# Optimization experiments

Measured on AMD Instinct MI355X. Metric: run time of the kernel, lower is better.

The kernel has to match this reference:

```python
import jax, jax.numpy as jnp
import numpy as np

N = 100000
IN_DIM = 128
HID = 64
OUT = 4


def _gcn_conv(x, W, b, src, dst, deg_inv_sqrt):
    """PyG GCNConv: linear transform, then symmetric-normalized scatter-add.
    src/dst already include self-loops; deg_inv_sqrt precomputed over them."""
    h = x @ W                                   # [N, H]
    norm = deg_inv_sqrt[src] * deg_inv_sqrt[dst]  # [E+N]
    msg = h[src] * norm[:, None]                # gather + scale, [E+N, H]
    out = jax.ops.segment_sum(msg, dst, num_segments=N)  # scatter-add
    return out + b


def setup_inputs() -> dict:
    key = jax.random.key(0)
    ks = jax.random.split(key, 8)
    E = 1600000
    x = jax.random.normal(ks[0], (N, IN_DIM), dtype=jnp.float32)
    edge_index = jax.random.randint(ks[1], (2, E), 0, N, dtype=jnp.int32)
    # Glorot-ish init for weights
    W1 = jax.random.normal(ks[2], (IN_DIM, HID), dtype=jnp.float32) / np.sqrt(IN_DIM)
    b1 = jnp.zeros((HID,), dtype=jnp.float32)
    W2 = jax.random.normal(ks[3], (HID, HID), dtype=jnp.float32) / np.sqrt(HID)
    b2 = jnp.zeros((HID,), dtype=jnp.float32)
    Wfc = jax.random.normal(ks[4], (HID, OUT), dtype=jnp.float32) / np.sqrt(HID)
    bfc = jnp.zeros((OUT,), dtype=jnp.float32)
    return {"x": x, "edge_index": edge_index, "W1": W1, "b1": b1,
            "W2": W2, "b2": b2, "Wfc": Wfc, "bfc": bfc}


def reference(x, edge_index, W1, b1, W2, b2, Wfc, bfc):
    # Add self-loops (GCNConv default add_self_loops=True)
    loops = jnp.arange(N, dtype=edge_index.dtype)
    src = jnp.concatenate([edge_index[0], loops])
    dst = jnp.concatenate([edge_index[1], loops])
    # Symmetric normalization: deg computed at aggregation targets (dst)
    deg = jax.ops.segment_sum(jnp.ones_like(dst, dtype=x.dtype), dst,
                              num_segments=N)
    deg_inv_sqrt = jnp.where(deg > 0, jax.lax.rsqrt(deg), 0.0)

    h = _gcn_conv(x, W1, b1, src, dst, deg_inv_sqrt)
    h = jax.nn.relu(h)                 # dropout is identity in eval mode
    h = _gcn_conv(h, W2, b2, src, dst, deg_inv_sqrt)
    h = jax.nn.relu(h)
    return h @ Wfc + bfc               # [N, 4]
```

## Files before the change

kernel.cpp:

```cpp
#include <hip/hip_runtime.h>
#include <hip/hip_fp16.h>


#define BCAP 5120
#define BINB 512
#define CHUNK 3200
#define CAP  64
#define LCAP 32

typedef float v2f __attribute__((ext_vector_type(2)));
typedef _Float16 f16x8 __attribute__((ext_vector_type(8)));
typedef float f32x4 __attribute__((ext_vector_type(4)));

__global__ __launch_bounds__(256) void k_bin_gemm1(
        const int* __restrict__ src, const int* __restrict__ dst, int e,
        int* bcur, unsigned* __restrict__ binned,
        const float* __restrict__ X, const float* __restrict__ W1,
        __half* __restrict__ Hh, int n) {
    __shared__ union {
        struct {
            unsigned ec[CHUNK];
            unsigned short eb[CHUNK];
            int lh[512], lbase[512], lr[512];
        } b;
        struct {
            _Float16 As[128 * 136];
            _Float16 Bs[64 * 136];
        } g;
    } sm;

    int t = threadIdx.x;

    if (blockIdx.x < BINB) {
        unsigned* ec = sm.b.ec;
        unsigned short* eb = sm.b.eb;
        int* lh = sm.b.lh; int* lbase = sm.b.lbase; int* lr = sm.b.lr;
        for (int i = t; i < 512; i += 256) { lh[i] = 0; lr[i] = 0; }
        __syncthreads();
        int chunk = (e + BINB - 1) / BINB;
        int lo = blockIdx.x * chunk;
        int hi = min(e, lo + chunk);
        for (int i = lo + t; i < hi; i += 256) {
            int d = dst[i];
            int b = d >> 8;
            ec[i - lo] = ((unsigned)src[i] << 8) | (unsigned)(d & 255);
            eb[i - lo] = (unsigned short)b;
            atomicAdd(&lh[b], 1);
        }
        __syncthreads();
        for (int i = t; i < 512; i += 256)
            lbase[i] = lh[i] ? atomicAdd(&bcur[i], lh[i]) : 0;
        __syncthreads();
        int cnt = hi - lo;
        for (int i = t; i < cnt; i += 256) {
            int b = eb[i];
            int r = lbase[b] + atomicAdd(&lr[b], 1);
            if (r < BCAP)
                binned[(size_t)b * BCAP + r] = ec[i];
        }
    } else {
        constexpr int K = 128, KP = 136;
        _Float16* As = sm.g.As;
        _Float16* Bs = sm.g.Bs;
        _Float16* H = (_Float16*)Hh;

        #pragma unroll
        for (int p = 0; p < 8; ++p) {
            int i = t + p * 256;
            int k = i >> 4, nn4 = (i & 15) << 2;
            float4 v = ((const float4*)W1)[i];
            Bs[(nn4 + 0) * KP + k] = (_Float16)v.x;
            Bs[(nn4 + 1) * KP + k] = (_Float16)v.y;
            Bs[(nn4 + 2) * KP + k] = (_Float16)v.z;
            Bs[(nn4 + 3) * KP + k] = (_Float16)v.w;
        }

        int row0 = (blockIdx.x - BINB) * 128;
        #pragma unroll
        for (int p = 0; p < 8; ++p) {
            int gi  = t + p * 256;
            int row = gi >> 4, sg = gi & 15;
            int grow = row0 + row;
            float4 v0 = make_float4(0.f, 0.f, 0.f, 0.f), v1 = v0;
            if (grow < n) {
                v0 = *(const float4*)(X + (size_t)grow * K + sg * 8);
                v1 = *(const float4*)(X + (size_t)grow * K + sg * 8 + 4);
            }
            union { __half2 h[4]; float4 f; } u;
            u.h[0] = __floats2half2_rn(v0.x, v0.y);
            u.h[1] = __floats2half2_rn(v0.z, v0.w);
            u.h[2] = __floats2half2_rn(v1.x, v1.y);
            u.h[3] = __floats2half2_rn(v1.z, v1.w);
            *(float4*)(As + row * KP + sg * 8) = u.f;
        }
        __syncthreads();

        int wv   = t >> 6;
        int lane = t & 63;
        int m    = lane & 15;
        int quad = lane >> 4;
        int r0   = wv * 32;

        f32x4 acc[2][4] = {};
        #pragma unroll
        for (int kb = 0; kb < K / 32; ++kb) {
            f16x8 af0 = *(const f16x8*)(As + (r0 + m) * KP + quad * 8 + kb * 32);
            f16x8 af1 = *(const f16x8*)(As + (r0 + 16 + m) * KP + quad * 8 + kb * 32);
            #pragma unroll
            for (int nt = 0; nt < 4; ++nt) {
                f16x8 bf = *(const f16x8*)(Bs + (nt * 16 + m) * KP + quad * 8 + kb * 32);
                acc[0][nt] = __builtin_amdgcn_mfma_f32_16x16x32_f16(af0, bf, acc[0][nt], 0, 0, 0);
                acc[1][nt] = __builtin_amdgcn_mfma_f32_16x16x32_f16(af1, bf, acc[1][nt], 0, 0, 0);
            }
        }

        #pragma unroll
        for (int mt = 0; mt < 2; ++mt) {
            int gr[4];
            #pragma unroll
            for (int r = 0; r < 4; ++r)
                gr[r] = row0 + r0 + mt * 16 + quad * 4 + r;
            #pragma unroll
            for (int nt = 0; nt < 4; ++nt)
                #pragma unroll
                for (int r = 0; r < 4; ++r) {
                    if (gr[r] < n)
                        H[(size_t)gr[r] * 64 + nt * 16 + m] =
                            (_Float16)acc[mt][nt][r];
                    else if (gr[r] == n)
                        H[(size_t)n * 64 + nt * 16 + m] = (_Float16)0.f;
                }
        }
    }
}

__global__ __launch_bounds__(256) void k_bucket2(const unsigned* __restrict__ binned,
                                                 const int* __restrict__ bcur,
                                                 int n, int* __restrict__ cnt,
                                                 int* __restrict__ slots) {
    __shared__ int lists[256 * (LCAP + 1)];
    __shared__ int lcnt[256];
    int b = blockIdx.x, t = threadIdx.x;
    int node0 = b << 8;
    size_t ebase = (size_t)b * BCAP;
    int ecnt = min(bcur[b], BCAP);
    lcnt[t] = 0;
    __syncthreads();
    for (int j = t; j < ecnt; j += 256) {
        unsigned ed = binned[ebase + j];
        int ld = ed & 255u;
        int s  = (int)(ed >> 8);
        int r  = atomicAdd(&lcnt[ld], 1);
        if (r < LCAP)
            lists[ld * (LCAP + 1) + r] = s;
        else if (r < CAP)
            slots[((size_t)(node0 + ld) << 6) + r] = s;
    }
    __syncthreads();
    int d = node0 + t;
    if (d < n) {
        int c = lcnt[t];
        cnt[d] = c;
        int m = min(c, LCAP);
        size_t base = (size_t)d << 6;
        for (int r = 0; r < m; ++r)
            slots[base + r] = lists[t * (LCAP + 1) + r];
    }
}

__global__ __launch_bounds__(256) void k_gemm2(const __half* __restrict__ X,
                                               const float* __restrict__ W2,
                                               const int* __restrict__ cnt,
                                               __half* __restrict__ Hh, int n) {
    constexpr int K = 64, KP = 72;
    __shared__ _Float16 As[128 * KP];
    __shared__ _Float16 Bs[64 * KP];

    int t = threadIdx.x;
    _Float16* H = (_Float16*)Hh;

    #pragma unroll
    for (int p = 0; p < 4; ++p) {
        int i = t + p * 256;
        int k = i >> 4, nn4 = (i & 15) << 2;
        float4 v = ((const float4*)W2)[i];
        Bs[(nn4 + 0) * KP + k] = (_Float16)v.x;
        Bs[(nn4 + 1) * KP + k] = (_Float16)v.y;
        Bs[(nn4 + 2) * KP + k] = (_Float16)v.z;
        Bs[(nn4 + 3) * KP + k] = (_Float16)v.w;
    }

    int row0 = blockIdx.x * 128;
    const __half* Xh = X;
    #pragma unroll
    for (int p = 0; p < 4; ++p) {
        int gi  = t + p * 256;
        int row = gi >> 3, sg = gi & 7;
        int grow = row0 + row;
        float4 v = make_float4(0.f, 0.f, 0.f, 0.f);
        if (grow < n)
            v = *(const float4*)(Xh + (size_t)grow * K + sg * 8);
        *(float4*)(As + row * KP + sg * 8) = v;
    }
    __syncthreads();

    int wv   = t >> 6;
    int lane = t & 63;
    int m    = lane & 15;
    int quad = lane >> 4;
    int r0   = wv * 32;

    f32x4 acc[2][4] = {};
    #pragma unroll
    for (int kb = 0; kb < K / 32; ++kb) {
        f16x8 af0 = *(const f16x8*)(As + (r0 + m) * KP + quad * 8 + kb * 32);
        f16x8 af1 = *(const f16x8*)(As + (r0 + 16 + m) * KP + quad * 8 + kb * 32);
        #pragma unroll
        for (int nt = 0; nt < 4; ++nt) {
            f16x8 bf = *(const f16x8*)(Bs + (nt * 16 + m) * KP + quad * 8 + kb * 32);
            acc[0][nt] = __builtin_amdgcn_mfma_f32_16x16x32_f16(af0, bf, acc[0][nt], 0, 0, 0);
            acc[1][nt] = __builtin_amdgcn_mfma_f32_16x16x32_f16(af1, bf, acc[1][nt], 0, 0, 0);
        }
    }

    #pragma unroll
    for (int mt = 0; mt < 2; ++mt) {
        float dv[4]; int gr[4];
        #pragma unroll
        for (int r = 0; r < 4; ++r) {
            gr[r] = row0 + r0 + mt * 16 + quad * 4 + r;
            dv[r] = (gr[r] < n) ? rsqrtf((float)(cnt[gr[r]] + 1)) : 0.f;
        }
        #pragma unroll
        for (int nt = 0; nt < 4; ++nt)
            #pragma unroll
            for (int r = 0; r < 4; ++r) {
                if (gr[r] < n)
                    H[(size_t)gr[r] * 64 + nt * 16 + m] =
                        (_Float16)(acc[mt][nt][r] * dv[r]);
                else if (gr[r] == n)
                    H[(size_t)n * 64 + nt * 16 + m] = (_Float16)0.f;
            }
    }
}

__device__ inline void add_row(const __half* __restrict__ hp, int s, int c4,
                               v2f& lo, v2f& hi) {
    float2 raw = *(const float2*)(hp + (size_t)s * 64 + c4);
    const __half2* p = (const __half2*)&raw;
    float2 l = __half22float2(p[0]);
    float2 h = __half22float2(p[1]);
    lo += (v2f){ l.x, l.y };
    hi += (v2f){ h.x, h.y };
}

__device__ inline void fma_row(const __half* __restrict__ hp, int s, int c4,
                               float w, v2f& lo, v2f& hi) {
    float2 raw = *(const float2*)(hp + (size_t)s * 64 + c4);
    const __half2* p = (const __half2*)&raw;
    float2 l = __half22float2(p[0]);
    float2 h = __half22float2(p[1]);
    lo += w * (v2f){ l.x, l.y };
    hi += w * (v2f){ h.x, h.y };
}

template<bool FUSE, bool SCALE>
__global__ __launch_bounds__(256) void k_gather(const __half* __restrict__ hp,
                                                const int* __restrict__ slots,
                                                const int* __restrict__ cnt,
                                                const float* __restrict__ bias,
                                                void* __restrict__ outb,
                                                const float* __restrict__ Wfc,
                                                const float* __restrict__ bfc,
                                                int n) {
    int lane = threadIdx.x & 63;
    int wid  = (blockIdx.x * blockDim.x + threadIdx.x) >> 6;
    if (wid >= n) return;
    int d    = wid;
    int esub = lane >> 4;
    int c4   = (lane & 15) * 4;

    size_t start = (size_t)d << 6;
    int num = cnt[d];
    int lim = min(num, CAP);
    int idx = (lane < lim) ? slots[start + lane] : 0;
    float dsv = 0.f;
    if constexpr (SCALE)
        dsv = rsqrtf((float)(cnt[idx] + 1));
    float dd = rsqrtf((float)(num + 1));

    v2f aL[4] = {}, aH[4] = {};
    if (esub == 0) {
        if constexpr (SCALE) fma_row(hp, d, c4, dd, aL[0], aH[0]);
        else                 add_row(hp, d, c4, aL[0], aH[0]);
    }

    int j = 0;
    for (; j + 16 <= lim; j += 16) {
        int s0 = __shfl(idx, j + esub);
        int s1 = __shfl(idx, j + 4 + esub);
        int s2 = __shfl(idx, j + 8 + esub);
        int s3 = __shfl(idx, j + 12 + esub);
        if constexpr (SCALE) {
            float w0 = __shfl(dsv, j + esub);
            float w1 = __shfl(dsv, j + 4 + esub);
            float w2 = __shfl(dsv, j + 8 + esub);
            float w3 = __shfl(dsv, j + 12 + esub);
            fma_row(hp, s0, c4, w0, aL[0], aH[0]);
            fma_row(hp, s1, c4, w1, aL[1], aH[1]);
            fma_row(hp, s2, c4, w2, aL[2], aH[2]);
            fma_row(hp, s3, c4, w3, aL[3], aH[3]);
        } else {
            add_row(hp, s0, c4, aL[0], aH[0]);
            add_row(hp, s1, c4, aL[1], aH[1]);
            add_row(hp, s2, c4, aL[2], aH[2]);
            add_row(hp, s3, c4, aL[3], aH[3]);
        }
    }
    for (; j < lim; j += 4) {
        int jj = j + esub;
        int sr = __shfl(idx, jj);
        int s  = (jj < lim) ? sr : n;
        if constexpr (SCALE) {
            float w = __shfl(dsv, jj);
            fma_row(hp, s, c4, w, aL[0], aH[0]);
        } else {
            add_row(hp, s, c4, aL[0], aH[0]);
        }
    }
    v2f sL = (aL[0] + aL[1]) + (aL[2] + aL[3]);
    v2f sH = (aH[0] + aH[1]) + (aH[2] + aH[3]);
    float4 a0 = make_float4(sL.x, sL.y, sH.x, sH.y);
    #pragma unroll
    for (int o = 16; o <= 32; o <<= 1) {
        a0.x += __shfl_xor(a0.x, o);
        a0.y += __shfl_xor(a0.y, o);
        a0.z += __shfl_xor(a0.z, o);
        a0.w += __shfl_xor(a0.w, o);
    }
    float4 bb = *(const float4*)(bias + c4);
    float4 o;
    o.x = fmaxf(bb.x + dd * a0.x, 0.f);
    o.y = fmaxf(bb.y + dd * a0.y, 0.f);
    o.z = fmaxf(bb.z + dd * a0.z, 0.f);
    o.w = fmaxf(bb.w + dd * a0.w, 0.f);
    if (!FUSE) {
        if (esub == 0) {
            union { __half2 h[2]; float2 f; } u;
            u.h[0] = __floats2half2_rn(o.x, o.y);
            u.h[1] = __floats2half2_rn(o.z, o.w);
            *(float2*)((__half*)outb + (size_t)d * 64 + c4) = u.f;
        }
    } else {
        const float4* W4 = (const float4*)Wfc;
        float4 w0 = W4[c4 + 0], w1 = W4[c4 + 1], w2 = W4[c4 + 2], w3 = W4[c4 + 3];
        float4 p;
        p.x = o.x * w0.x + o.y * w1.x + o.z * w2.x + o.w * w3.x;
        p.y = o.x * w0.y + o.y * w1.y + o.z * w2.y + o.w * w3.y;
        p.z = o.x * w0.z + o.y * w1.z + o.z * w2.z + o.w * w3.z;
        p.w = o.x * w0.w + o.y * w1.w + o.z * w2.w + o.w * w3.w;
        #pragma unroll
        for (int q = 1; q <= 8; q <<= 1) {
            p.x += __shfl_xor(p.x, q);
            p.y += __shfl_xor(p.y, q);
            p.z += __shfl_xor(p.z, q);
            p.w += __shfl_xor(p.w, q);
        }
        if (lane == 0) {
            float4 bf = *(const float4*)bfc;
            float4 r = make_float4(p.x + bf.x, p.y + bf.y, p.z + bf.z, p.w + bf.w);
            ((float4*)outb)[d] = r;
        }
    }
}

static inline size_t align256(size_t x) { return (x + 255) & ~(size_t)255; }

extern "C" void kernel_launch(void* const* d_in, const int* in_sizes, int n_in,
                              void* d_out, int out_size, void* d_ws, size_t ws_size,
                              hipStream_t stream) {
    const float* x   = (const float*)d_in[0];
    const int*   ei  = (const int*)d_in[1];
    const float* W1  = (const float*)d_in[2];
    const float* b1  = (const float*)d_in[3];
    const float* W2  = (const float*)d_in[4];
    const float* b2  = (const float*)d_in[5];
    const float* Wfc = (const float*)d_in[6];
    const float* bfc = (const float*)d_in[7];
    float* out = (float*)d_out;

    int n = in_sizes[0] / 128;
    int e = in_sizes[1] / 2;
    const int* src = ei;
    const int* dst = ei + e;

    char* ws = (char*)d_ws;
    size_t p = 0;
    int*      cnt    = (int*)     (ws + p); p = align256(p + (size_t)n * 4);
    int*      bcur   = (int*)     (ws + p); p = align256(p + 512 * 4);
    unsigned* binned = (unsigned*)(ws + p); p = align256(p + (size_t)512 * BCAP * 4);
    int*      slots  = (int*)     (ws + p); p = align256(p + (size_t)n * CAP * 4);
    __half*   hbuf   = (__half*)  (ws + p); p = align256(p + (size_t)(n + 1) * 64 * 2);
    __half*   a1h    = (__half*)  (ws + p);

    int gb  = (n + 127) / 128;
    int nbk = (n + 255) / 256;

    hipMemsetAsync(bcur, 0, 512 * sizeof(int), stream);
    k_bin_gemm1<<<BINB + gb, 256, 0, stream>>>(src, dst, e, bcur, binned,
                                               x, W1, hbuf, n);
    k_bucket2<<<nbk, 256, 0, stream>>>(binned, bcur, n, cnt, slots);

    k_gather<false, true><<<(n * 64 + 255) / 256, 256, 0, stream>>>(
        hbuf, slots, cnt, b1, a1h, nullptr, nullptr, n);

    k_gemm2<<<gb, 256, 0, stream>>>(a1h, W2, cnt, hbuf, n);
    k_gather<true, false><<<(n * 64 + 255) / 256, 256, 0, stream>>>(
        hbuf, slots, cnt, b2, out, Wfc, bfc, n);
}
```

Before: 253.3 us.

## Fuse second GEMM into first gather and co-schedule bucketing with GEMM1

Splits binning into its own kernel and merges the per-node bucket pass with the first GEMM in one grid. The layer-2 linear transform moves into the first gather kernel: each wave loads W2 into 64 registers and does a shuffle-based 64x64 matvec per node, writing pre-scaled fp16 H2. This drops the separate k_gemm2 launch and the round trip of the intermediate activation through memory. The cost is heavy per-thread register use (64 floats of W2 plus the accumulators) and scalar FMA work where MFMA was used before, which may lower occupancy in a latency-bound gather.

```diff
diff --git a/kernel.cpp b/kernel.cpp
--- a/kernel.cpp
+++ b/kernel.cpp
@@ -12,17 +12,48 @@
 typedef _Float16 f16x8 __attribute__((ext_vector_type(8)));
 typedef float f32x4 __attribute__((ext_vector_type(4)));
 
-__global__ __launch_bounds__(256) void k_bin_gemm1(
-        const int* __restrict__ src, const int* __restrict__ dst, int e,
-        int* bcur, unsigned* __restrict__ binned,
+__global__ __launch_bounds__(256) void k_bin(const int* __restrict__ src,
+                                             const int* __restrict__ dst, int e,
+                                             int* bcur, unsigned* __restrict__ binned) {
+    __shared__ unsigned ec[CHUNK];
+    __shared__ unsigned short eb[CHUNK];
+    __shared__ int lh[512], lbase[512], lr[512];
+    int t = threadIdx.x;
+    for (int i = t; i < 512; i += 256) { lh[i] = 0; lr[i] = 0; }
+    __syncthreads();
+    int chunk = (e + BINB - 1) / BINB;
+    int lo = blockIdx.x * chunk;
+    int hi = min(e, lo + chunk);
+    for (int i = lo + t; i < hi; i += 256) {
+        int d = dst[i];
+        int b = d >> 8;
+        ec[i - lo] = ((unsigned)src[i] << 8) | (unsigned)(d & 255);
+        eb[i - lo] = (unsigned short)b;
+        atomicAdd(&lh[b], 1);
+    }
+    __syncthreads();
+    for (int i = t; i < 512; i += 256)
+        lbase[i] = lh[i] ? atomicAdd(&bcur[i], lh[i]) : 0;
+    __syncthreads();
+    int cnt = hi - lo;
+    for (int i = t; i < cnt; i += 256) {
+        int b = eb[i];
+        int r = lbase[b] + atomicAdd(&lr[b], 1);
+        if (r < BCAP)
+            binned[(size_t)b * BCAP + r] = ec[i];
+    }
+}
+
+__global__ __launch_bounds__(256) void k_bk2_gemm1(
+        const unsigned* __restrict__ binned, const int* __restrict__ bcur,
+        int nbk, int* __restrict__ cnt, int* __restrict__ slots,
         const float* __restrict__ X, const float* __restrict__ W1,
         __half* __restrict__ Hh, int n) {
     __shared__ union {
         struct {
-            unsigned ec[CHUNK];
-            unsigned short eb[CHUNK];
-            int lh[512], lbase[512], lr[512];
-        } b;
+            int lists[256 * (LCAP + 1)];
+            int lcnt[256];
+        } k;
         struct {
             _Float16 As[128 * 136];
             _Float16 Bs[64 * 136];
@@ -31,32 +62,31 @@
 
     int t = threadIdx.x;
 
-    if (blockIdx.x < BINB) {
-        unsigned* ec = sm.b.ec;
-        unsigned short* eb = sm.b.eb;
-        int* lh = sm.b.lh; int* lbase = sm.b.lbase; int* lr = sm.b.lr;
-        for (int i = t; i < 512; i += 256) { lh[i] = 0; lr[i] = 0; }
+    if ((int)blockIdx.x < nbk) {
+        int b = blockIdx.x;
+        int node0 = b << 8;
+        size_t ebase = (size_t)b * BCAP;
+        int ecnt = min(bcur[b], BCAP);
+        sm.k.lcnt[t] = 0;
         __syncthreads();
-        int chunk = (e + BINB - 1) / BINB;
-        int lo = blockIdx.x * chunk;
-        int hi = min(e, lo + chunk);
-        for (int i = lo + t; i < hi; i += 256) {
-            int d = dst[i];
-            int b = d >> 8;
-            ec[i - lo] = ((unsigned)src[i] << 8) | (unsigned)(d & 255);
-            eb[i - lo] = (unsigned short)b;
-            atomicAdd(&lh[b], 1);
+        for (int j = t; j < ecnt; j += 256) {
+            unsigned ed = binned[ebase + j];
+            int ld = ed & 255u;
+            int s  = (int)(ed >> 8);
+            int r  = atomicAdd(&sm.k.lcnt[ld], 1);
+            if (r < LCAP)
+                sm.k.lists[ld * (LCAP + 1) + r] = s;
+            else if (r < CAP)
+                slots[((size_t)(node0 + ld) << 6) + r] = s;
         }
         __syncthreads();
-        for (int i = t; i < 512; i += 256)
-            lbase[i] = lh[i] ? atomicAdd(&bcur[i], lh[i]) : 0;
-        __syncthreads();
-        int cnt = hi - lo;
-        for (int i = t; i < cnt; i += 256) {
-            int b = eb[i];
-            int r = lbase[b] + atomicAdd(&lr[b], 1);
-            if (r < BCAP)
-                binned[(size_t)b * BCAP + r] = ec[i];
+        if (node0 + t < n) cnt[node0 + t] = sm.k.lcnt[t];
+        for (int k = t; k < 256 * LCAP; k += 256) {
+            int ld = k >> 5;
+            int r  = k & (LCAP - 1);
+            if (r < min(sm.k.lcnt[ld], LCAP) && node0 + ld < n)
+                slots[((size_t)(node0 + ld) << 6) + r] =
+                    sm.k.lists[ld * (LCAP + 1) + r];
         }
     } else {
         constexpr int K = 128, KP = 136;
@@ -75,7 +105,7 @@
             Bs[(nn4 + 3) * KP + k] = (_Float16)v.w;
         }
 
-        int row0 = (blockIdx.x - BINB) * 128;
+        int row0 = ((int)blockIdx.x - nbk) * 128;
         #pragma unroll
         for (int p = 0; p < 8; ++p) {
             int gi  = t + p * 256;
@@ -134,116 +164,6 @@
     }
 }
 
-__global__ __launch_bounds__(256) void k_bucket2(const unsigned* __restrict__ binned,
-                                                 const int* __restrict__ bcur,
-                                                 int n, int* __restrict__ cnt,
-                                                 int* __restrict__ slots) {
-    __shared__ int lists[256 * (LCAP + 1)];
-    __shared__ int lcnt[256];
-    int b = blockIdx.x, t = threadIdx.x;
-    int node0 = b << 8;
-    size_t ebase = (size_t)b * BCAP;
-    int ecnt = min(bcur[b], BCAP);
-    lcnt[t] = 0;
-    __syncthreads();
-    for (int j = t; j < ecnt; j += 256) {
-        unsigned ed = binned[ebase + j];
-        int ld = ed & 255u;
-        int s  = (int)(ed >> 8);
-        int r  = atomicAdd(&lcnt[ld], 1);
-        if (r < LCAP)
-            lists[ld * (LCAP + 1) + r] = s;
-        else if (r < CAP)
-            slots[((size_t)(node0 + ld) << 6) + r] = s;
-    }
-    __syncthreads();
-    int d = node0 + t;
-    if (d < n) {
-        int c = lcnt[t];
-        cnt[d] = c;
-        int m = min(c, LCAP);
-        size_t base = (size_t)d << 6;
-        for (int r = 0; r < m; ++r)
-            slots[base + r] = lists[t * (LCAP + 1) + r];
-    }
-}
-
-__global__ __launch_bounds__(256) void k_gemm2(const __half* __restrict__ X,
-                                               const float* __restrict__ W2,
-                                               const int* __restrict__ cnt,
-                                               __half* __restrict__ Hh, int n) {
-    constexpr int K = 64, KP = 72;
-    __shared__ _Float16 As[128 * KP];
-    __shared__ _Float16 Bs[64 * KP];
-
-    int t = threadIdx.x;
-    _Float16* H = (_Float16*)Hh;
-
-    #pragma unroll
-    for (int p = 0; p < 4; ++p) {
-        int i = t + p * 256;
-        int k = i >> 4, nn4 = (i & 15) << 2;
-        float4 v = ((const float4*)W2)[i];
-        Bs[(nn4 + 0) * KP + k] = (_Float16)v.x;
-        Bs[(nn4 + 1) * KP + k] = (_Float16)v.y;
-        Bs[(nn4 + 2) * KP + k] = (_Float16)v.z;
-        Bs[(nn4 + 3) * KP + k] = (_Float16)v.w;
-    }
-
-    int row0 = blockIdx.x * 128;
-    const __half* Xh = X;
-    #pragma unroll
-    for (int p = 0; p < 4; ++p) {
-        int gi  = t + p * 256;
-        int row = gi >> 3, sg = gi & 7;
-        int grow = row0 + row;
-        float4 v = make_float4(0.f, 0.f, 0.f, 0.f);
-        if (grow < n)
-            v = *(const float4*)(Xh + (size_t)grow * K + sg * 8);
-        *(float4*)(As + row * KP + sg * 8) = v;
-    }
-    __syncthreads();
-
-    int wv   = t >> 6;
-    int lane = t & 63;
-    int m    = lane & 15;
-    int quad = lane >> 4;
-    int r0   = wv * 32;
-
-    f32x4 acc[2][4] = {};
-    #pragma unroll
-    for (int kb = 0; kb < K / 32; ++kb) {
-        f16x8 af0 = *(const f16x8*)(As + (r0 + m) * KP + quad * 8 + kb * 32);
-        f16x8 af1 = *(const f16x8*)(As + (r0 + 16 + m) * KP + quad * 8 + kb * 32);
-        #pragma unroll
-        for (int nt = 0; nt < 4; ++nt) {
-            f16x8 bf = *(const f16x8*)(Bs + (nt * 16 + m) * KP + quad * 8 + kb * 32);
-            acc[0][nt] = __builtin_amdgcn_mfma_f32_16x16x32_f16(af0, bf, acc[0][nt], 0, 0, 0);
-            acc[1][nt] = __builtin_amdgcn_mfma_f32_16x16x32_f16(af1, bf, acc[1][nt], 0, 0, 0);
-        }
-    }
-
-    #pragma unroll
-    for (int mt = 0; mt < 2; ++mt) {
-        float dv[4]; int gr[4];
-        #pragma unroll
-        for (int r = 0; r < 4; ++r) {
-            gr[r] = row0 + r0 + mt * 16 + quad * 4 + r;
-            dv[r] = (gr[r] < n) ? rsqrtf((float)(cnt[gr[r]] + 1)) : 0.f;
-        }
-        #pragma unroll
-        for (int nt = 0; nt < 4; ++nt)
-            #pragma unroll
-            for (int r = 0; r < 4; ++r) {
-                if (gr[r] < n)
-                    H[(size_t)gr[r] * 64 + nt * 16 + m] =
-                        (_Float16)(acc[mt][nt][r] * dv[r]);
-                else if (gr[r] == n)
-                    H[(size_t)n * 64 + nt * 16 + m] = (_Float16)0.f;
-            }
-    }
-}
-
 __device__ inline void add_row(const __half* __restrict__ hp, int s, int c4,
                                v2f& lo, v2f& hi) {
     float2 raw = *(const float2*)(hp + (size_t)s * 64 + c4);
@@ -264,15 +184,13 @@
     hi += w * (v2f){ h.x, h.y };
 }
 
-template<bool FUSE, bool SCALE>
-__global__ __launch_bounds__(256) void k_gather(const __half* __restrict__ hp,
-                                                const int* __restrict__ slots,
-                                                const int* __restrict__ cnt,
-                                                const float* __restrict__ bias,
-                                                void* __restrict__ outb,
-                                                const float* __restrict__ Wfc,
-                                                const float* __restrict__ bfc,
-                                                int n) {
+__global__ __launch_bounds__(256) void k_gather_mm(const __half* __restrict__ hp,
+                                                   const int* __restrict__ slots,
+                                                   const int* __restrict__ cnt,
+                                                   const float* __restrict__ bias,
+                                                   const float* __restrict__ W2,
+                                                   __half* __restrict__ h2,
+                                                   int n) {
     int lane = threadIdx.x & 63;
     int wid  = (blockIdx.x * blockDim.x + threadIdx.x) >> 6;
     if (wid >= n) return;
@@ -280,20 +198,21 @@
     int esub = lane >> 4;
     int c4   = (lane & 15) * 4;
 
+    float w[64];
+    #pragma unroll
+    for (int k = 0; k < 64; ++k)
+        w[k] = W2[k * 64 + lane];
+
     size_t start = (size_t)d << 6;
     int num = cnt[d];
     int lim = min(num, CAP);
     int idx = (lane < lim) ? slots[start + lane] : 0;
-    float dsv = 0.f;
-    if constexpr (SCALE)
-        dsv = rsqrtf((float)(cnt[idx] + 1));
-    float dd = rsqrtf((float)(num + 1));
+    float dsv = rsqrtf((float)(cnt[idx] + 1));
+    float dd  = rsqrtf((float)(num + 1));
 
     v2f aL[4] = {}, aH[4] = {};
-    if (esub == 0) {
-        if constexpr (SCALE) fma_row(hp, d, c4, dd, aL[0], aH[0]);
-        else                 add_row(hp, d, c4, aL[0], aH[0]);
-    }
+    if (esub == 0)
+        fma_row(hp, d, c4, dd, aL[0], aH[0]);
 
     int j = 0;
     for (; j + 16 <= lim; j += 16) {
@@ -301,32 +220,21 @@
         int s1 = __shfl(idx, j + 4 + esub);
         int s2 = __shfl(idx, j + 8 + esub);
         int s3 = __shfl(idx, j + 12 + esub);
-        if constexpr (SCALE) {
-            float w0 = __shfl(dsv, j + esub);
-            float w1 = __shfl(dsv, j + 4 + esub);
-            float w2 = __shfl(dsv, j + 8 + esub);
-            float w3 = __shfl(dsv, j + 12 + esub);
-            fma_row(hp, s0, c4, w0, aL[0], aH[0]);
-            fma_row(hp, s1, c4, w1, aL[1], aH[1]);
-            fma_row(hp, s2, c4, w2, aL[2], aH[2]);
-            fma_row(hp, s3, c4, w3, aL[3], aH[3]);
-        } else {
-            add_row(hp, s0, c4, aL[0], aH[0]);
-            add_row(hp, s1, c4, aL[1], aH[1]);
-            add_row(hp, s2, c4, aL[2], aH[2]);
-            add_row(hp, s3, c4, aL[3], aH[3]);
-        }
+        float w0 = __shfl(dsv, j + esub);
+        float w1 = __shfl(dsv, j + 4 + esub);
+        float w2 = __shfl(dsv, j + 8 + esub);
+        float w3 = __shfl(dsv, j + 12 + esub);
+        fma_row(hp, s0, c4, w0, aL[0], aH[0]);
+        fma_row(hp, s1, c4, w1, aL[1], aH[1]);
+        fma_row(hp, s2, c4, w2, aL[2], aH[2]);
+        fma_row(hp, s3, c4, w3, aL[3], aH[3]);
     }
     for (; j < lim; j += 4) {
         int jj = j + esub;
         int sr = __shfl(idx, jj);
         int s  = (jj < lim) ? sr : n;
-        if constexpr (SCALE) {
-            float w = __shfl(dsv, jj);
-            fma_row(hp, s, c4, w, aL[0], aH[0]);
-        } else {
-            add_row(hp, s, c4, aL[0], aH[0]);
-        }
+        float ww = __shfl(dsv, jj);
+        fma_row(hp, s, c4, ww, aL[0], aH[0]);
     }
     v2f sL = (aL[0] + aL[1]) + (aL[2] + aL[3]);
     v2f sH = (aH[0] + aH[1]) + (aH[2] + aH[3]);
@@ -344,33 +252,102 @@
     o.y = fmaxf(bb.y + dd * a0.y, 0.f);
     o.z = fmaxf(bb.z + dd * a0.z, 0.f);
     o.w = fmaxf(bb.w + dd * a0.w, 0.f);
-    if (!FUSE) {
-        if (esub == 0) {
-            union { __half2 h[2]; float2 f; } u;
-            u.h[0] = __floats2half2_rn(o.x, o.y);
-            u.h[1] = __floats2half2_rn(o.z, o.w);
-            *(float2*)((__half*)outb + (size_t)d * 64 + c4) = u.f;
-        }
-    } else {
-        const float4* W4 = (const float4*)Wfc;
-        float4 w0 = W4[c4 + 0], w1 = W4[c4 + 1], w2 = W4[c4 + 2], w3 = W4[c4 + 3];
-        float4 p;
-        p.x = o.x * w0.x + o.y * w1.x + o.z * w2.x + o.w * w3.x;
-        p.y = o.x * w0.y + o.y * w1.y + o.z * w2.y + o.w * w3.y;
-        p.z = o.x * w0.z + o.y * w1.z + o.z * w2.z + o.w * w3.z;
-        p.w = o.x * w0.w + o.y * w1.w + o.z * w2.w + o.w * w3.w;
-        #pragma unroll
-        for (int q = 1; q <= 8; q <<= 1) {
-            p.x += __shfl_xor(p.x, q);
-            p.y += __shfl_xor(p.y, q);
-            p.z += __shfl_xor(p.z, q);
-            p.w += __shfl_xor(p.w, q);
-        }
-        if (lane == 0) {
-            float4 bf = *(const float4*)bfc;
-            float4 r = make_float4(p.x + bf.x, p.y + bf.y, p.z + bf.z, p.w + bf.w);
-            ((float4*)outb)[d] = r;
-        }
+
+    float s = 0.f;
+    #pragma unroll
+    for (int kq = 0; kq < 16; ++kq) {
+        float ax = __shfl(o.x, kq);
+        float ay = __shfl(o.y, kq);
+        float az = __shfl(o.z, kq);
+        float aw = __shfl(o.w, kq);
+        s += ax * w[4 * kq + 0];
+        s += ay * w[4 * kq + 1];
+        s += az * w[4 * kq + 2];
+        s += aw * w[4 * kq + 3];
+    }
+    _Float16* h2f = (_Float16*)h2;
+    h2f[(size_t)d * 64 + lane] = (_Float16)(s * dd);
+    if (wid == 0)
+        h2f[(size_t)n * 64 + lane] = (_Float16)0.f;
+}
+
+__global__ __launch_bounds__(256) void k_gather_fc(const __half* __restrict__ hp,
+                                                   const int* __restrict__ slots,
+                                                   const int* __restrict__ cnt,
+                                                   const float* __restrict__ bias,
+                                                   float* __restrict__ outb,
+                                                   const float* __restrict__ Wfc,
+                                                   const float* __restrict__ bfc,
+                                                   int n) {
+    int lane = threadIdx.x & 63;
+    int wid  = (blockIdx.x * blockDim.x + threadIdx.x) >> 6;
+    if (wid >= n) return;
+    int d    = wid;
+    int esub = lane >> 4;
+    int c4   = (lane & 15) * 4;
+
+    size_t start = (size_t)d << 6;
+    int num = cnt[d];
+    int lim = min(num, CAP);
+    int idx = (lane < lim) ? slots[start + lane] : 0;
+    float dd = rsqrtf((float)(num + 1));
+
+    v2f aL[4] = {}, aH[4] = {};
+    if (esub == 0)
+        add_row(hp, d, c4, aL[0], aH[0]);
+
+    int j = 0;
+    for (; j + 16 <= lim; j += 16) {
+        int s0 = __shfl(idx, j + esub);
+        int s1 = __shfl(idx, j + 4 + esub);
+        int s2 = __shfl(idx, j + 8 + esub);
+        int s3 = __shfl(idx, j + 12 + esub);
+        add_row(hp, s0, c4, aL[0], aH[0]);
+        add_row(hp, s1, c4, aL[1], aH[1]);
+        add_row(hp, s2, c4, aL[2], aH[2]);
+        add_row(hp, s3, c4, aL[3], aH[3]);
+    }
+    for (; j < lim; j += 4) {
+        int jj = j + esub;
+        int sr = __shfl(idx, jj);
+        int s  = (jj < lim) ? sr : n;
+        add_row(hp, s, c4, aL[0], aH[0]);
+    }
+    v2f sL = (aL[0] + aL[1]) + (aL[2] + aL[3]);
+    v2f sH = (aH[0] + aH[1]) + (aH[2] + aH[3]);
+    float4 a0 = make_float4(sL.x, sL.y, sH.x, sH.y);
+    #pragma unroll
+    for (int o = 16; o <= 32; o <<= 1) {
+        a0.x += __shfl_xor(a0.x, o);
+        a0.y += __shfl_xor(a0.y, o);
+        a0.z += __shfl_xor(a0.z, o);
+        a0.w += __shfl_xor(a0.w, o);
+    }
+    float4 bb = *(const float4*)(bias + c4);
+    float4 o;
+    o.x = fmaxf(bb.x + dd * a0.x, 0.f);
+    o.y = fmaxf(bb.y + dd * a0.y, 0.f);
+    o.z = fmaxf(bb.z + dd * a0.z, 0.f);
+    o.w = fmaxf(bb.w + dd * a0.w, 0.f);
+
+    const float4* W4 = (const float4*)Wfc;
+    float4 w0 = W4[c4 + 0], w1 = W4[c4 + 1], w2 = W4[c4 + 2], w3 = W4[c4 + 3];
+    float4 p;
+    p.x = o.x * w0.x + o.y * w1.x + o.z * w2.x + o.w * w3.x;
+    p.y = o.x * w0.y + o.y * w1.y + o.z * w2.y + o.w * w3.y;
+    p.z = o.x * w0.z + o.y * w1.z + o.z * w2.z + o.w * w3.z;
+    p.w = o.x * w0.w + o.y * w1.w + o.z * w2.w + o.w * w3.w;
+    #pragma unroll
+    for (int q = 1; q <= 8; q <<= 1) {
+        p.x += __shfl_xor(p.x, q);
+        p.y += __shfl_xor(p.y, q);
+        p.z += __shfl_xor(p.z, q);
+        p.w += __shfl_xor(p.w, q);
+    }
+    if (lane == 0) {
+        float4 bf = *(const float4*)bfc;
+        float4 r = make_float4(p.x + bf.x, p.y + bf.y, p.z + bf.z, p.w + bf.w);
+        ((float4*)outb)[d] = r;
     }
 }
 
@@ -401,20 +378,19 @@
     unsigned* binned = (unsigned*)(ws + p); p = align256(p + (size_t)512 * BCAP * 4);
     int*      slots  = (int*)     (ws + p); p = align256(p + (size_t)n * CAP * 4);
     __half*   hbuf   = (__half*)  (ws + p); p = align256(p + (size_t)(n + 1) * 64 * 2);
-    __half*   a1h    = (__half*)  (ws + p);
+    __half*   hbuf2  = (__half*)  (ws + p); p = align256(p + (size_t)(n + 1) * 64 * 2);
 
     int gb  = (n + 127) / 128;
     int nbk = (n + 255) / 256;
 
     hipMemsetAsync(bcur, 0, 512 * sizeof(int), stream);
-    k_bin_gemm1<<<BINB + gb, 256, 0, stream>>>(src, dst, e, bcur, binned,
-                                               x, W1, hbuf, n);
-    k_bucket2<<<nbk, 256, 0, stream>>>(binned, bcur, n, cnt, slots);
-
-    k_gather<false, true><<<(n * 64 + 255) / 256, 256, 0, stream>>>(
-        hbuf, slots, cnt, b1, a1h, nullptr, nullptr, n);
-
-    k_gemm2<<<gb, 256, 0, stream>>>(a1h, W2, cnt, hbuf, n);
-    k_gather<true, false><<<(n * 64 + 255) / 256, 256, 0, stream>>>(
-        hbuf, slots, cnt, b2, out, Wfc, bfc, n);
-}
+    k_bin<<<BINB, 256, 0, stream>>>(src, dst, e, bcur, binned);
+    k_bk2_gemm1<<<nbk + gb, 256, 0, stream>>>(binned, bcur, nbk, cnt, slots,
+                                              x, W1, hbuf, n);
+
+    k_gather_mm<<<(n * 64 + 255) / 256, 256, 0, stream>>>(
+        hbuf, slots, cnt, b1, W2, hbuf2, n);
+
+    k_gather_fc<<<(n * 64 + 255) / 256, 256, 0, stream>>>(
+        hbuf2, slots, cnt, b2, out, Wfc, bfc, n);
+}
```

New measurement: 309.2 us. 22.1% more time.

## Fuse bucket pass with first GEMM and split gathers into two launches

Applied to the files above, without the earlier changes.

Edge binning now runs as its own kernel, and the per-bucket list-building pass is merged into the same launch as the first dense transform. Previously the transform was fused with binning. The transform does not depend on the graph, so its blocks can overlap with bucket processing instead of with binning. The bucket pass's slot writes are also restructured so that consecutive threads write consecutive slot entries, which coalesces the stores. Each gather kernel is split into two launches covering halves of the node range. This adds launch overhead, and the purpose of the split is unclear.

```diff
diff --git a/kernel.cpp b/kernel.cpp
--- a/kernel.cpp
+++ b/kernel.cpp
@@ -12,17 +12,48 @@
 typedef _Float16 f16x8 __attribute__((ext_vector_type(8)));
 typedef float f32x4 __attribute__((ext_vector_type(4)));
 
-__global__ __launch_bounds__(256) void k_bin_gemm1(
-        const int* __restrict__ src, const int* __restrict__ dst, int e,
-        int* bcur, unsigned* __restrict__ binned,
+__global__ __launch_bounds__(256) void k_bin(const int* __restrict__ src,
+                                             const int* __restrict__ dst, int e,
+                                             int* bcur, unsigned* __restrict__ binned) {
+    __shared__ unsigned ec[CHUNK];
+    __shared__ unsigned short eb[CHUNK];
+    __shared__ int lh[512], lbase[512], lr[512];
+    int t = threadIdx.x;
+    for (int i = t; i < 512; i += 256) { lh[i] = 0; lr[i] = 0; }
+    __syncthreads();
+    int chunk = (e + BINB - 1) / BINB;
+    int lo = blockIdx.x * chunk;
+    int hi = min(e, lo + chunk);
+    for (int i = lo + t; i < hi; i += 256) {
+        int d = dst[i];
+        int b = d >> 8;
+        ec[i - lo] = ((unsigned)src[i] << 8) | (unsigned)(d & 255);
+        eb[i - lo] = (unsigned short)b;
+        atomicAdd(&lh[b], 1);
+    }
+    __syncthreads();
+    for (int i = t; i < 512; i += 256)
+        lbase[i] = lh[i] ? atomicAdd(&bcur[i], lh[i]) : 0;
+    __syncthreads();
+    int cnt = hi - lo;
+    for (int i = t; i < cnt; i += 256) {
+        int b = eb[i];
+        int r = lbase[b] + atomicAdd(&lr[b], 1);
+        if (r < BCAP)
+            binned[(size_t)b * BCAP + r] = ec[i];
+    }
+}
+
+__global__ __launch_bounds__(256) void k_bk2_gemm1(
+        const unsigned* __restrict__ binned, const int* __restrict__ bcur,
+        int nbk, int* __restrict__ cnt, int* __restrict__ slots,
         const float* __restrict__ X, const float* __restrict__ W1,
         __half* __restrict__ Hh, int n) {
     __shared__ union {
         struct {
-            unsigned ec[CHUNK];
-            unsigned short eb[CHUNK];
-            int lh[512], lbase[512], lr[512];
-        } b;
+            int lists[256 * (LCAP + 1)];
+            int lcnt[256];
+        } k;
         struct {
             _Float16 As[128 * 136];
             _Float16 Bs[64 * 136];
@@ -31,32 +62,31 @@
 
     int t = threadIdx.x;
 
-    if (blockIdx.x < BINB) {
-        unsigned* ec = sm.b.ec;
-        unsigned short* eb = sm.b.eb;
-        int* lh = sm.b.lh; int* lbase = sm.b.lbase; int* lr = sm.b.lr;
-        for (int i = t; i < 512; i += 256) { lh[i] = 0; lr[i] = 0; }
+    if ((int)blockIdx.x < nbk) {
+        int b = blockIdx.x;
+        int node0 = b << 8;
+        size_t ebase = (size_t)b * BCAP;
+        int ecnt = min(bcur[b], BCAP);
+        sm.k.lcnt[t] = 0;
         __syncthreads();
-        int chunk = (e + BINB - 1) / BINB;
-        int lo = blockIdx.x * chunk;
-        int hi = min(e, lo + chunk);
-        for (int i = lo + t; i < hi; i += 256) {
-            int d = dst[i];
-            int b = d >> 8;
-            ec[i - lo] = ((unsigned)src[i] << 8) | (unsigned)(d & 255);
-            eb[i - lo] = (unsigned short)b;
-            atomicAdd(&lh[b], 1);
+        for (int j = t; j < ecnt; j += 256) {
+            unsigned ed = binned[ebase + j];
+            int ld = ed & 255u;
+            int s  = (int)(ed >> 8);
+            int r  = atomicAdd(&sm.k.lcnt[ld], 1);
+            if (r < LCAP)
+                sm.k.lists[ld * (LCAP + 1) + r] = s;
+            else if (r < CAP)
+                slots[((size_t)(node0 + ld) << 6) + r] = s;
         }
         __syncthreads();
-        for (int i = t; i < 512; i += 256)
-            lbase[i] = lh[i] ? atomicAdd(&bcur[i], lh[i]) : 0;
-        __syncthreads();
-        int cnt = hi - lo;
-        for (int i = t; i < cnt; i += 256) {
-            int b = eb[i];
-            int r = lbase[b] + atomicAdd(&lr[b], 1);
-            if (r < BCAP)
-                binned[(size_t)b * BCAP + r] = ec[i];
+        if (node0 + t < n) cnt[node0 + t] = sm.k.lcnt[t];
+        for (int k = t; k < 256 * LCAP; k += 256) {
+            int ld = k >> 5;
+            int r  = k & (LCAP - 1);
+            if (r < min(sm.k.lcnt[ld], LCAP) && node0 + ld < n)
+                slots[((size_t)(node0 + ld) << 6) + r] =
+                    sm.k.lists[ld * (LCAP + 1) + r];
         }
     } else {
         constexpr int K = 128, KP = 136;
@@ -75,7 +105,7 @@
             Bs[(nn4 + 3) * KP + k] = (_Float16)v.w;
         }
 
-        int row0 = (blockIdx.x - BINB) * 128;
+        int row0 = ((int)blockIdx.x - nbk) * 128;
         #pragma unroll
         for (int p = 0; p < 8; ++p) {
             int gi  = t + p * 256;
@@ -134,40 +164,6 @@
     }
 }
 
-__global__ __launch_bounds__(256) void k_bucket2(const unsigned* __restrict__ binned,
-                                                 const int* __restrict__ bcur,
-                                                 int n, int* __restrict__ cnt,
-                                                 int* __restrict__ slots) {
-    __shared__ int lists[256 * (LCAP + 1)];
-    __shared__ int lcnt[256];
-    int b = blockIdx.x, t = threadIdx.x;
-    int node0 = b << 8;
-    size_t ebase = (size_t)b * BCAP;
-    int ecnt = min(bcur[b], BCAP);
-    lcnt[t] = 0;
-    __syncthreads();
-    for (int j = t; j < ecnt; j += 256) {
-        unsigned ed = binned[ebase + j];
-        int ld = ed & 255u;
-        int s  = (int)(ed >> 8);
-        int r  = atomicAdd(&lcnt[ld], 1);
-        if (r < LCAP)
-            lists[ld * (LCAP + 1) + r] = s;
-        else if (r < CAP)
-            slots[((size_t)(node0 + ld) << 6) + r] = s;
-    }
-    __syncthreads();
-    int d = node0 + t;
-    if (d < n) {
-        int c = lcnt[t];
-        cnt[d] = c;
-        int m = min(c, LCAP);
-        size_t base = (size_t)d << 6;
-        for (int r = 0; r < m; ++r)
-            slots[base + r] = lists[t * (LCAP + 1) + r];
-    }
-}
-
 __global__ __launch_bounds__(256) void k_gemm2(const __half* __restrict__ X,
                                                const float* __restrict__ W2,
                                                const int* __restrict__ cnt,
@@ -272,10 +268,10 @@
                                                 void* __restrict__ outb,
                                                 const float* __restrict__ Wfc,
                                                 const float* __restrict__ bfc,
-                                                int n) {
+                                                int wid0, int wlim, int n) {
     int lane = threadIdx.x & 63;
-    int wid  = (blockIdx.x * blockDim.x + threadIdx.x) >> 6;
-    if (wid >= n) return;
+    int wid  = wid0 + ((blockIdx.x * blockDim.x + threadIdx.x) >> 6);
+    if (wid >= wlim) return;
     int d    = wid;
     int esub = lane >> 4;
     int c4   = (lane & 15) * 4;
@@ -407,14 +403,21 @@
     int nbk = (n + 255) / 256;
 
     hipMemsetAsync(bcur, 0, 512 * sizeof(int), stream);
-    k_bin_gemm1<<<BINB + gb, 256, 0, stream>>>(src, dst, e, bcur, binned,
-                                               x, W1, hbuf, n);
-    k_bucket2<<<nbk, 256, 0, stream>>>(binned, bcur, n, cnt, slots);
-
-    k_gather<false, true><<<(n * 64 + 255) / 256, 256, 0, stream>>>(
-        hbuf, slots, cnt, b1, a1h, nullptr, nullptr, n);
+    k_bin<<<BINB, 256, 0, stream>>>(src, dst, e, bcur, binned);
+    k_bk2_gemm1<<<nbk + gb, 256, 0, stream>>>(binned, bcur, nbk, cnt, slots,
+                                              x, W1, hbuf, n);
+
+    int halfw = (n + 1) / 2;
+    int hgrid = (halfw * 64 + 255) / 256;
+
+    k_gather<false, true><<<hgrid, 256, 0, stream>>>(
+        hbuf, slots, cnt, b1, a1h, nullptr, nullptr, 0, halfw, n);
+    k_gather<false, true><<<hgrid, 256, 0, stream>>>(
+        hbuf, slots, cnt, b1, a1h, nullptr, nullptr, halfw, n, n);
 
     k_gemm2<<<gb, 256, 0, stream>>>(a1h, W2, cnt, hbuf, n);
-    k_gather<true, false><<<(n * 64 + 255) / 256, 256, 0, stream>>>(
-        hbuf, slots, cnt, b2, out, Wfc, bfc, n);
-}
+    k_gather<true, false><<<hgrid, 256, 0, stream>>>(
+        hbuf, slots, cnt, b2, out, Wfc, bfc, 0, halfw, n);
+    k_gather<true, false><<<hgrid, 256, 0, stream>>>(
+        hbuf, slots, cnt, b2, out, Wfc, bfc, halfw, n, n);
+}
```

Measured after the change: 261.6 us. 1.03x slower.

## Locally sort edges by bin before writing, compute degrees with global atomics

Applied to the files above, without the earlier changes.

The binning blocks now do a local counting sort: they histogram bins, prefix-scan them, and place edges into shared memory ordered by bin. The binned output is then written in contiguous runs instead of scattered single words. Per-node degree counts are now built with global atomicAdd during the histogram pass, which removes the cnt write from the bucket kernel. The bucket kernel's slot copy is also restructured so threads write consecutive slots for coalescing. The cost is 1.6M extra global atomics, a second read of dst, and a larger memset.

```diff
diff --git a/kernel.cpp b/kernel.cpp
--- a/kernel.cpp
+++ b/kernel.cpp
@@ -14,14 +14,14 @@
 
 __global__ __launch_bounds__(256) void k_bin_gemm1(
         const int* __restrict__ src, const int* __restrict__ dst, int e,
-        int* bcur, unsigned* __restrict__ binned,
+        int* bcur, unsigned* __restrict__ binned, int* __restrict__ cnt,
         const float* __restrict__ X, const float* __restrict__ W1,
         __half* __restrict__ Hh, int n) {
     __shared__ union {
         struct {
-            unsigned ec[CHUNK];
-            unsigned short eb[CHUNK];
-            int lh[512], lbase[512], lr[512];
+            unsigned sorted[CHUNK];
+            unsigned short sortedb[CHUNK];
+            int lh[512], lscan[512], lbase[512], lr[512], nsc[256];
         } b;
         struct {
             _Float16 As[128 * 136];
@@ -31,32 +31,50 @@
 
     int t = threadIdx.x;
 
-    if (blockIdx.x < BINB) {
-        unsigned* ec = sm.b.ec;
-        unsigned short* eb = sm.b.eb;
-        int* lh = sm.b.lh; int* lbase = sm.b.lbase; int* lr = sm.b.lr;
-        for (int i = t; i < 512; i += 256) { lh[i] = 0; lr[i] = 0; }
+    if ((int)blockIdx.x < BINB) {
+        auto& B = sm.b;
+        for (int i = t; i < 512; i += 256) { B.lh[i] = 0; B.lr[i] = 0; }
         __syncthreads();
         int chunk = (e + BINB - 1) / BINB;
         int lo = blockIdx.x * chunk;
         int hi = min(e, lo + chunk);
         for (int i = lo + t; i < hi; i += 256) {
             int d = dst[i];
+            atomicAdd(&B.lh[d >> 8], 1);
+            atomicAdd(&cnt[d], 1);
+        }
+        __syncthreads();
+        int a0 = B.lh[2 * t], a1 = B.lh[2 * t + 1];
+        int s = a0 + a1;
+        B.nsc[t] = s;
+        __syncthreads();
+        for (int o = 1; o < 256; o <<= 1) {
+            int x = (t >= o) ? B.nsc[t - o] : 0;
+            __syncthreads();
+            B.nsc[t] += x;
+            __syncthreads();
+        }
+        int ex = B.nsc[t] - s;
+        B.lscan[2 * t]     = ex;
+        B.lscan[2 * t + 1] = ex + a0;
+        B.lbase[2 * t]     = a0 ? atomicAdd(&bcur[2 * t],     a0) : 0;
+        B.lbase[2 * t + 1] = a1 ? atomicAdd(&bcur[2 * t + 1], a1) : 0;
+        __syncthreads();
+        for (int i = lo + t; i < hi; i += 256) {
+            int d = dst[i];
             int b = d >> 8;
-            ec[i - lo] = ((unsigned)src[i] << 8) | (unsigned)(d & 255);
-            eb[i - lo] = (unsigned short)b;
-            atomicAdd(&lh[b], 1);
-        }
-        __syncthreads();
-        for (int i = t; i < 512; i += 256)
-            lbase[i] = lh[i] ? atomicAdd(&bcur[i], lh[i]) : 0;
-        __syncthreads();
-        int cnt = hi - lo;
-        for (int i = t; i < cnt; i += 256) {
-            int b = eb[i];
-            int r = lbase[b] + atomicAdd(&lr[b], 1);
-            if (r < BCAP)
-                binned[(size_t)b * BCAP + r] = ec[i];
+            int r = atomicAdd(&B.lr[b], 1);
+            int pos = B.lscan[b] + r;
+            B.sorted[pos]  = ((unsigned)src[i] << 8) | (unsigned)(d & 255);
+            B.sortedb[pos] = (unsigned short)b;
+        }
+        __syncthreads();
+        int m = hi - lo;
+        for (int i = t; i < m; i += 256) {
+            int b = B.sortedb[i];
+            int off = B.lbase[b] + (i - B.lscan[b]);
+            if (off < BCAP)
+                binned[(size_t)b * BCAP + off] = B.sorted[i];
         }
     } else {
         constexpr int K = 128, KP = 136;
@@ -75,7 +93,7 @@
             Bs[(nn4 + 3) * KP + k] = (_Float16)v.w;
         }
 
-        int row0 = (blockIdx.x - BINB) * 128;
+        int row0 = ((int)blockIdx.x - BINB) * 128;
         #pragma unroll
         for (int p = 0; p < 8; ++p) {
             int gi  = t + p * 256;
@@ -136,8 +154,7 @@
 
 __global__ __launch_bounds__(256) void k_bucket2(const unsigned* __restrict__ binned,
                                                  const int* __restrict__ bcur,
-                                                 int n, int* __restrict__ cnt,
-                                                 int* __restrict__ slots) {
+                                                 int n, int* __restrict__ slots) {
     __shared__ int lists[256 * (LCAP + 1)];
     __shared__ int lcnt[256];
     int b = blockIdx.x, t = threadIdx.x;
@@ -157,14 +174,12 @@
             slots[((size_t)(node0 + ld) << 6) + r] = s;
     }
     __syncthreads();
-    int d = node0 + t;
-    if (d < n) {
-        int c = lcnt[t];
-        cnt[d] = c;
-        int m = min(c, LCAP);
-        size_t base = (size_t)d << 6;
-        for (int r = 0; r < m; ++r)
-            slots[base + r] = lists[t * (LCAP + 1) + r];
+    for (int k = t; k < 256 * LCAP; k += 256) {
+        int ld = k >> 5;
+        int r  = k & (LCAP - 1);
+        if (r < min(lcnt[ld], LCAP) && node0 + ld < n)
+            slots[((size_t)(node0 + ld) << 6) + r] =
+                lists[ld * (LCAP + 1) + r];
     }
 }
 
@@ -397,7 +412,8 @@
     char* ws = (char*)d_ws;
     size_t p = 0;
     int*      cnt    = (int*)     (ws + p); p = align256(p + (size_t)n * 4);
-    int*      bcur   = (int*)     (ws + p); p = align256(p + 512 * 4);
+    int*      bcur   = (int*)     (ws + p); size_t zend = p + 512 * 4;
+    p = align256(zend);
     unsigned* binned = (unsigned*)(ws + p); p = align256(p + (size_t)512 * BCAP * 4);
     int*      slots  = (int*)     (ws + p); p = align256(p + (size_t)n * CAP * 4);
     __half*   hbuf   = (__half*)  (ws + p); p = align256(p + (size_t)(n + 1) * 64 * 2);
@@ -406,10 +422,10 @@
     int gb  = (n + 127) / 128;
     int nbk = (n + 255) / 256;
 
-    hipMemsetAsync(bcur, 0, 512 * sizeof(int), stream);
-    k_bin_gemm1<<<BINB + gb, 256, 0, stream>>>(src, dst, e, bcur, binned,
+    hipMemsetAsync(ws, 0, zend, stream);
+    k_bin_gemm1<<<BINB + gb, 256, 0, stream>>>(src, dst, e, bcur, binned, cnt,
                                                x, W1, hbuf, n);
-    k_bucket2<<<nbk, 256, 0, stream>>>(binned, bcur, n, cnt, slots);
+    k_bucket2<<<nbk, 256, 0, stream>>>(binned, bcur, n, slots);
 
     k_gather<false, true><<<(n * 64 + 255) / 256, 256, 0, stream>>>(
         hbuf, slots, cnt, b1, a1h, nullptr, nullptr, n);
```

Result: slower. 318.5 us (+25.7%).
